# Optimization experiments

Measured on AMD Instinct MI355X. Metric: run time of the kernel, lower is better.

Reference implementation:

```python
import jax, jax.numpy as jnp
import numpy as np

B, S, D = 8, 4096, 1024  # batch, seq, input_dim == hidden_dim


def setup_inputs() -> dict:
    key = jax.random.key(0)
    k1, k2, k3, k4, k5 = jax.random.split(key, 5)
    s = 1.0 / np.sqrt(D)
    return {
        "q": jax.random.normal(k1, (B, S, D), dtype=jnp.float32),
        "k": jax.random.normal(k2, (B, D), dtype=jnp.float32),
        # torch Linear(in,out,bias=False) weight is [out,in]; store transposed [in,out]
        "W1": jax.random.uniform(k3, (D, D), dtype=jnp.float32, minval=-s, maxval=s),
        "W2": jax.random.uniform(k4, (D, D), dtype=jnp.float32, minval=-s, maxval=s),
        "V": jax.random.uniform(k5, (D, D), dtype=jnp.float32, minval=-s, maxval=s),
    }


def reference(q, k, W1, W2, V):
    # q: [B,S,D], k: [B,D]
    h_q = jnp.einsum("bsd,dh->bsh", q, W1)          # W1(q): [B,S,H]
    h_k = jnp.einsum("bd,dh->bh", k, W2)[:, None]   # W2(k).unsqueeze(1): [B,1,H]
    scores = jnp.einsum("bsh,hv->bsv", jnp.tanh(h_q + h_k), V)  # [B,S,H]
    weights = jax.nn.softmax(scores, axis=-1)       # softmax over feature dim (as in source)
    values = jnp.sum(weights * q, axis=1)           # [B,D]
    return values, weights
```

## Files before the change

### kernel.cpp

```cpp
#include <hip/hip_runtime.h>
#include <hip/hip_bf16.h>

#define DDIM 1024
#define BATCH 8
#define SEQ 4096
#define MROWS (BATCH*SEQ)

typedef __attribute__((ext_vector_type(8))) short short8;
typedef __attribute__((ext_vector_type(4))) float floatx4;

__device__ inline short f2bf(float f) {
    unsigned int u = __builtin_bit_cast(unsigned int, f);
    unsigned int r = (u + 0x7fffu + ((u >> 16) & 1u)) >> 16;
    return (short)r;
}
__device__ inline float bf2f(short s) {
    unsigned int u = ((unsigned int)(unsigned short)s) << 16;
    return __builtin_bit_cast(float, u);
}

__device__ inline float fast_tanh(float x) {
    float e = __expf(2.f * x);
    return 1.f - 2.f / (e + 1.f);
}

typedef const __attribute__((address_space(1))) unsigned int* gas_ptr;
typedef __attribute__((address_space(3))) unsigned int* las_ptr;
__device__ __forceinline__ void gl16(const short* g, short* l) {
    __builtin_amdgcn_global_load_lds((gas_ptr)g, (las_ptr)l, 16, 0, 0);
}

#define VMCNT4 asm volatile("s_waitcnt vmcnt(4)" ::: "memory")
#define VMCNT0 asm volatile("s_waitcnt vmcnt(0)" ::: "memory")
#define BARRIER do { __builtin_amdgcn_sched_barrier(0); __builtin_amdgcn_s_barrier(); \
                     __builtin_amdgcn_sched_barrier(0); } while (0)

__global__ __launch_bounds__(256) void prep_kernel(const float* __restrict__ q,
                                                   short* __restrict__ qb,
                                                   const float* __restrict__ W1,
                                                   short* __restrict__ W1T,
                                                   const float* __restrict__ V,
                                                   short* __restrict__ VT,
                                                   const float* __restrict__ k,
                                                   const float* __restrict__ W2,
                                                   float* __restrict__ hk) {
    int bid = blockIdx.x;
    if (bid < 2048) {
        size_t t = (size_t)bid * 256 + threadIdx.x;
        const size_t stride = (size_t)2048 * 256;
        for (int it = 0; it < 8; ++it, t += stride) {
            size_t i = t * 8;
            float4 f0 = *(const float4*)(q + i);
            float4 f1 = *(const float4*)(q + i + 4);
            short8 v;
            v[0]=f2bf(f0.x); v[1]=f2bf(f0.y); v[2]=f2bf(f0.z); v[3]=f2bf(f0.w);
            v[4]=f2bf(f1.x); v[5]=f2bf(f1.y); v[6]=f2bf(f1.z); v[7]=f2bf(f1.w);
            *(short8*)(qb + i) = v;
        }
    } else if (bid < 4096) {
        const float* src = (bid < 3072) ? W1 : V;
        short* dst = (bid < 3072) ? W1T : VT;
        int tb = (bid - 2048) & 1023;
        __shared__ float t[32][33];
        int bx = tb & 31, by = tb >> 5;
        int c  = threadIdx.x & 31;
        int r0 = threadIdx.x >> 5;
        for (int p = 0; p < 4; ++p) {
            int r = p * 8 + r0;
            t[r][c] = src[(size_t)(by * 32 + r) * DDIM + bx * 32 + c];
        }
        __syncthreads();
        for (int p = 0; p < 4; ++p) {
            int r = p * 8 + r0;
            dst[(size_t)(bx * 32 + r) * DDIM + by * 32 + c] = f2bf(t[c][r]);
        }
    } else {
        int hb = bid - 4096;
        int b  = hb >> 4;
        int h0 = (hb & 15) * 64;
        int hl = threadIdx.x & 63;
        int dc = threadIdx.x >> 6;
        const float* kb = k + (size_t)b * DDIM;
        float sum = 0.f;
        for (int d = dc * 256; d < dc * 256 + 256; ++d)
            sum += kb[d] * W2[(size_t)d * DDIM + h0 + hl];
        __shared__ float red[4][64];
        red[dc][hl] = sum;
        __syncthreads();
        if (dc == 0)
            hk[(size_t)b * DDIM + h0 + hl] = red[0][hl] + red[1][hl] + red[2][hl] + red[3][hl];
    }
}

template<int EPI>
__global__ __launch_bounds__(512, 2) void gemm256_kernel(const short* __restrict__ A,
                                                         const short* __restrict__ Bt,
                                                         const float* __restrict__ hk,
                                                         short* __restrict__ Out) {
    __shared__ __align__(16) short lds[2 * 32768];
    int bid = blockIdx.x;
    int swz = (bid & 7) * 64 + (bid >> 3);
    int mt = swz >> 2, nt = swz & 3;
    int m0 = mt * 256, n0 = nt * 256;
    int tid = threadIdx.x, lane = tid & 63, wid = tid >> 6;
    int wm = (wid >> 2) * 16;
    int wn = (wid & 3) * 16;
    int lr = lane & 15, kb = lane >> 4;
    floatx4 acc[8][4] = {};

    int srow = lane >> 3;
    int sblk = (lane & 7) ^ srow;
    const size_t arow_base = (size_t)(m0 + wid * 8 + srow) * DDIM + sblk * 8;
    const size_t brow_base = (size_t)(n0 + wid * 8 + srow) * DDIM + sblk * 8;
    const int lds_st = wid * 512 + lane * 8;

    auto stage = [&](int buf, int isB, int h, int t) {
        const short* src = isB ? Bt : A;
        size_t rb = isB ? brow_base : arow_base;
        #pragma unroll
        for (int r = 0; r < 2; ++r)
            gl16(src + rb + (size_t)(h * 128 + r * 64) * DDIM + t * 64,
                 lds + buf * 32768 + isB * 16384 + h * 8192 + r * 4096 + lds_st);
    };
    auto rdA = [&](int buf, int mi, int kk) -> short8 {
        int row = wm + mi * 32 + lr;
        return *(const short8*)(lds + buf * 32768 + (row >> 7) * 8192 +
                                (row & 127) * 64 + (((kk * 4 + kb) ^ (row & 7)) * 8));
    };
    auto rdB = [&](int buf, int ni, int kk) -> short8 {
        int row = wn + ni * 64 + lr;
        return *(const short8*)(lds + buf * 32768 + 16384 + (row >> 7) * 8192 +
                                (row & 127) * 64 + (((kk * 4 + kb) ^ (row & 7)) * 8));
    };

    stage(0, 0, 0, 0); stage(0, 1, 0, 0); stage(0, 1, 1, 0); stage(0, 0, 1, 0);
    VMCNT4;
    BARRIER;

    short8 a0[4][2], a1[4][2], b0[2][2], b1[2][2];

    for (int t = 0; t < 15; ++t) {
        int cb = t & 1, nb = cb ^ 1;
        stage(nb, 0, 0, t + 1);
        #pragma unroll
        for (int mi = 0; mi < 4; ++mi)
            #pragma unroll
            for (int kk = 0; kk < 2; ++kk) a0[mi][kk] = rdA(cb, mi, kk);
        #pragma unroll
        for (int ni = 0; ni < 2; ++ni)
            #pragma unroll
            for (int kk = 0; kk < 2; ++kk) b0[ni][kk] = rdB(cb, ni, kk);
        __builtin_amdgcn_s_setprio(1);
        #pragma unroll
        for (int mi = 0; mi < 4; ++mi)
            #pragma unroll
            for (int ni = 0; ni < 2; ++ni)
                #pragma unroll
                for (int kk = 0; kk < 2; ++kk)
                    acc[mi][ni] = __builtin_amdgcn_mfma_f32_16x16x32_bf16(a0[mi][kk], b0[ni][kk], acc[mi][ni], 0, 0, 0);
        __builtin_amdgcn_s_setprio(0);
        VMCNT4;
        BARRIER;
        stage(nb, 1, 0, t + 1);
        #pragma unroll
        for (int ni = 0; ni < 2; ++ni)
            #pragma unroll
            for (int kk = 0; kk < 2; ++kk) b1[ni][kk] = rdB(cb, ni + 2, kk);
        __builtin_amdgcn_s_setprio(1);
        #pragma unroll
        for (int mi = 0; mi < 4; ++mi)
            #pragma unroll
            for (int ni = 0; ni < 2; ++ni)
                #pragma unroll
                for (int kk = 0; kk < 2; ++kk)
                    acc[mi][ni + 2] = __builtin_amdgcn_mfma_f32_16x16x32_bf16(a0[mi][kk], b1[ni][kk], acc[mi][ni + 2], 0, 0, 0);
        __builtin_amdgcn_s_setprio(0);
        VMCNT4;
        BARRIER;
        stage(nb, 1, 1, t + 1);
        #pragma unroll
        for (int mi = 0; mi < 4; ++mi)
            #pragma unroll
            for (int kk = 0; kk < 2; ++kk) a1[mi][kk] = rdA(cb, mi + 4, kk);
        __builtin_amdgcn_s_setprio(1);
        #pragma unroll
        for (int mi = 0; mi < 4; ++mi)
            #pragma unroll
            for (int ni = 0; ni < 2; ++ni)
                #pragma unroll
                for (int kk = 0; kk < 2; ++kk)
                    acc[mi + 4][ni] = __builtin_amdgcn_mfma_f32_16x16x32_bf16(a1[mi][kk], b0[ni][kk], acc[mi + 4][ni], 0, 0, 0);
        __builtin_amdgcn_s_setprio(0);
        BARRIER;
        stage(nb, 0, 1, t + 1);
        __builtin_amdgcn_s_setprio(1);
        #pragma unroll
        for (int mi = 0; mi < 4; ++mi)
            #pragma unroll
            for (int ni = 0; ni < 2; ++ni)
                #pragma unroll
                for (int kk = 0; kk < 2; ++kk)
                    acc[mi + 4][ni + 2] = __builtin_amdgcn_mfma_f32_16x16x32_bf16(a1[mi][kk], b1[ni][kk], acc[mi + 4][ni + 2], 0, 0, 0);
        __builtin_amdgcn_s_setprio(0);
        VMCNT4;
        BARRIER;
    }

    {
        const int cb = 1;
        #pragma unroll
        for (int mi = 0; mi < 4; ++mi)
            #pragma unroll
            for (int kk = 0; kk < 2; ++kk) a0[mi][kk] = rdA(cb, mi, kk);
        #pragma unroll
        for (int ni = 0; ni < 2; ++ni)
            #pragma unroll
            for (int kk = 0; kk < 2; ++kk) b0[ni][kk] = rdB(cb, ni, kk);
        #pragma unroll
        for (int mi = 0; mi < 4; ++mi)
            #pragma unroll
            for (int ni = 0; ni < 2; ++ni)
                #pragma unroll
                for (int kk = 0; kk < 2; ++kk)
                    acc[mi][ni] = __builtin_amdgcn_mfma_f32_16x16x32_bf16(a0[mi][kk], b0[ni][kk], acc[mi][ni], 0, 0, 0);
        VMCNT0;
        BARRIER;
        #pragma unroll
        for (int ni = 0; ni < 2; ++ni)
            #pragma unroll
            for (int kk = 0; kk < 2; ++kk) b1[ni][kk] = rdB(cb, ni + 2, kk);
        #pragma unroll
        for (int mi = 0; mi < 4; ++mi)
            #pragma unroll
            for (int kk = 0; kk < 2; ++kk) a1[mi][kk] = rdA(cb, mi + 4, kk);
        #pragma unroll
        for (int mi = 0; mi < 4; ++mi)
            #pragma unroll
            for (int ni = 0; ni < 2; ++ni)
                #pragma unroll
                for (int kk = 0; kk < 2; ++kk) {
                    acc[mi][ni + 2]     = __builtin_amdgcn_mfma_f32_16x16x32_bf16(a0[mi][kk], b1[ni][kk], acc[mi][ni + 2], 0, 0, 0);
                    acc[mi + 4][ni]     = __builtin_amdgcn_mfma_f32_16x16x32_bf16(a1[mi][kk], b0[ni][kk], acc[mi + 4][ni], 0, 0, 0);
                    acc[mi + 4][ni + 2] = __builtin_amdgcn_mfma_f32_16x16x32_bf16(a1[mi][kk], b1[ni][kk], acc[mi + 4][ni + 2], 0, 0, 0);
                }
    }

    int rr = lane >> 4;
    if constexpr (EPI == 0) {
        int bidx = m0 >> 12;
        #pragma unroll
        for (int ni = 0; ni < 4; ++ni) {
            int col = n0 + wn + ni * 64 + lr;
            float hkv = hk[(size_t)bidx * DDIM + col];
            #pragma unroll
            for (int mi = 0; mi < 8; ++mi)
                #pragma unroll
                for (int j = 0; j < 4; ++j) {
                    int row = m0 + wm + mi * 32 + rr * 4 + j;
                    Out[(size_t)row * DDIM + col] = f2bf(fast_tanh(acc[mi][ni][j] + hkv));
                }
        }
    } else {
        #pragma unroll
        for (int ni = 0; ni < 4; ++ni) {
            int col = n0 + wn + ni * 64 + lr;
            #pragma unroll
            for (int mi = 0; mi < 8; ++mi)
                #pragma unroll
                for (int j = 0; j < 4; ++j) {
                    int row = m0 + wm + mi * 32 + rr * 4 + j;
                    Out[(size_t)row * DDIM + col] = f2bf(__expf(acc[mi][ni][j]));
                }
        }
    }
}

template<int QBF>
__global__ __launch_bounds__(256) void softmax_wsum_kernel(const short* __restrict__ E,
                                                           float* __restrict__ weights,
                                                           const float* __restrict__ q,
                                                           const short* __restrict__ qb,
                                                           float* __restrict__ partials) {
    int blk   = blockIdx.x;
    int b     = blk >> 8;
    int chunk = blk & 255;
    int tid   = threadIdx.x;
    int lane  = tid & 63, wid = tid >> 6;

    float pv[2][8] = {};
    size_t rowbase = ((size_t)b * SEQ + (size_t)chunk * 16 + (size_t)wid * 4) * DDIM;
    #pragma unroll 1
    for (int r = 0; r < 4; ++r) {
        const short* ep = E + rowbase + (size_t)r * DDIM;
        float x[2][8];
        float ls = 0.f;
        #pragma unroll
        for (int kk = 0; kk < 2; ++kk) {
            short8 v = *(const short8*)(ep + lane * 8 + kk * 512);
            #pragma unroll
            for (int j = 0; j < 8; ++j) { x[kk][j] = bf2f(v[j]); ls += x[kk][j]; }
        }
        #pragma unroll
        for (int o = 32; o > 0; o >>= 1) ls += __shfl_xor(ls, o);
        float inv = 1.f / ls;
        float* wp = weights + rowbase + (size_t)r * DDIM;
        #pragma unroll
        for (int kk = 0; kk < 2; ++kk) {
            int d = lane * 8 + kk * 512;
            float w[8];
            #pragma unroll
            for (int j = 0; j < 8; ++j) w[j] = x[kk][j] * inv;
            *(float4*)(wp + d)     = make_float4(w[0], w[1], w[2], w[3]);
            *(float4*)(wp + d + 4) = make_float4(w[4], w[5], w[6], w[7]);
            if constexpr (QBF) {
                short8 qv = *(const short8*)(qb + rowbase + (size_t)r * DDIM + d);
                #pragma unroll
                for (int j = 0; j < 8; ++j) pv[kk][j] += w[j] * bf2f(qv[j]);
            } else {
                const float* qp = q + rowbase + (size_t)r * DDIM;
                float4 q4a = *(const float4*)(qp + d);
                float4 q4b = *(const float4*)(qp + d + 4);
                pv[kk][0] += w[0] * q4a.x; pv[kk][1] += w[1] * q4a.y;
                pv[kk][2] += w[2] * q4a.z; pv[kk][3] += w[3] * q4a.w;
                pv[kk][4] += w[4] * q4b.x; pv[kk][5] += w[5] * q4b.y;
                pv[kk][6] += w[6] * q4b.z; pv[kk][7] += w[7] * q4b.w;
            }
        }
    }

    __shared__ float red[4][DDIM];
    #pragma unroll
    for (int kk = 0; kk < 2; ++kk) {
        int d = lane * 8 + kk * 512;
        *(float4*)(&red[wid][d])     = *(float4*)(&pv[kk][0]);
        *(float4*)(&red[wid][d + 4]) = *(float4*)(&pv[kk][4]);
    }
    __syncthreads();
    {
        int d = tid * 4;
        float4 s0 = *(float4*)(&red[0][d]);
        float4 s1 = *(float4*)(&red[1][d]);
        float4 s2 = *(float4*)(&red[2][d]);
        float4 s3 = *(float4*)(&red[3][d]);
        float4 o;
        o.x = s0.x + s1.x + s2.x + s3.x;
        o.y = s0.y + s1.y + s2.y + s3.y;
        o.z = s0.z + s1.z + s2.z + s3.z;
        o.w = s0.w + s1.w + s2.w + s3.w;
        *(float4*)(partials + (size_t)blk * DDIM + d) = o;
    }
}

__global__ __launch_bounds__(256) void reduce_values_kernel(const float* __restrict__ partials,
                                                            float* __restrict__ values) {
    int gid = blockIdx.x * 256 + threadIdx.x;
    int b = gid >> 10, v = gid & 1023;
    float s = 0.f;
    for (int c = 0; c < 256; ++c)
        s += partials[((size_t)b * 256 + c) * DDIM + v];
    values[gid] = s;
}

extern "C" void kernel_launch(void* const* d_in, const int* in_sizes, int n_in,
                              void* d_out, int out_size, void* d_ws, size_t ws_size,
                              hipStream_t stream) {
    const float* q  = (const float*)d_in[0];
    const float* k  = (const float*)d_in[1];
    const float* W1 = (const float*)d_in[2];
    const float* W2 = (const float*)d_in[3];
    const float* V  = (const float*)d_in[4];

    float* values  = (float*)d_out;
    float* weights = (float*)d_out + (size_t)BATCH * DDIM;

    const size_t hk_b   = (((size_t)BATCH * DDIM * 4) + 255) & ~(size_t)255;
    const size_t wT_b   = (size_t)DDIM * DDIM * 2;
    const size_t big_b  = (size_t)MROWS * DDIM * 2;
    const size_t part_b = (size_t)2048 * DDIM * 4;
    const size_t need_qbf_ws = hk_b + 2 * wT_b + 2 * big_b + part_b;

    char* ws = (char*)d_ws;
    float* hk  = (float*)ws;  ws += hk_b;
    short* W1T = (short*)ws;  ws += wT_b;
    short* VT  = (short*)ws;  ws += wT_b;
    short* E   = (short*)ws;  ws += big_b;

    short* q_bf;
    float* partials;
    bool qbf_in_ws = (ws_size >= need_qbf_ws);
    if (qbf_in_ws) {
        q_bf = (short*)ws;    ws += big_b;
        partials = (float*)ws;
    } else {
        q_bf = (short*)weights;
        partials = (float*)ws;
    }
    short* H = (short*)weights + (qbf_in_ws ? 0 : (size_t)MROWS * DDIM);

    prep_kernel<<<dim3(4224), dim3(256), 0, stream>>>(q, q_bf, W1, W1T, V, VT, k, W2, hk);
    gemm256_kernel<0><<<dim3(512), dim3(512), 0, stream>>>(q_bf, W1T, hk, H);
    gemm256_kernel<1><<<dim3(512), dim3(512), 0, stream>>>(H, VT, nullptr, E);
    if (qbf_in_ws)
        softmax_wsum_kernel<1><<<dim3(2048), dim3(256), 0, stream>>>(E, weights, q, q_bf, partials);
    else
        softmax_wsum_kernel<0><<<dim3(2048), dim3(256), 0, stream>>>(E, weights, q, q_bf, partials);
    reduce_values_kernel<<<dim3(32), dim3(256), 0, stream>>>(partials, values);
}
```

Measured before the change: 258.3 us.

## Fuse fp32-to-bf16 conversion of q into the first GEMM's A-tile loading

Removes the separate q bf16 conversion pass from the prep kernel. The first GEMM now loads fp32 q tiles into registers, converts them to bf16 and writes them into LDS itself. Blocks with nt==0 also store the converted tile to the q_bf buffer for later use by the softmax kernel. This saves one full read and write pass over q, but each A tile is read as fp32 four times (once per N tile), and the register-staged loads replace the async global-to-LDS path, which adds register pressure and changes pipelining.

Measured after the change: 269.4 us. +4.3%, slower.

```diff
diff --git a/kernel.cpp b/kernel.cpp
--- a/kernel.cpp
+++ b/kernel.cpp
@@ -18,6 +18,12 @@
     unsigned int u = ((unsigned int)(unsigned short)s) << 16;
     return __builtin_bit_cast(float, u);
 }
+__device__ inline short8 pack8(float4 a, float4 b) {
+    short8 v;
+    v[0]=f2bf(a.x); v[1]=f2bf(a.y); v[2]=f2bf(a.z); v[3]=f2bf(a.w);
+    v[4]=f2bf(b.x); v[5]=f2bf(b.y); v[6]=f2bf(b.z); v[7]=f2bf(b.w);
+    return v;
+}
 
 __device__ inline float fast_tanh(float x) {
     float e = __expf(2.f * x);
@@ -31,13 +37,13 @@
 }
 
 #define VMCNT4 asm volatile("s_waitcnt vmcnt(4)" ::: "memory")
+#define VMCNT6 asm volatile("s_waitcnt vmcnt(6)" ::: "memory")
 #define VMCNT0 asm volatile("s_waitcnt vmcnt(0)" ::: "memory")
+#define LGKM0  asm volatile("s_waitcnt lgkmcnt(0)" ::: "memory")
 #define BARRIER do { __builtin_amdgcn_sched_barrier(0); __builtin_amdgcn_s_barrier(); \
                      __builtin_amdgcn_sched_barrier(0); } while (0)
 
-__global__ __launch_bounds__(256) void prep_kernel(const float* __restrict__ q,
-                                                   short* __restrict__ qb,
-                                                   const float* __restrict__ W1,
+__global__ __launch_bounds__(256) void prep_kernel(const float* __restrict__ W1,
                                                    short* __restrict__ W1T,
                                                    const float* __restrict__ V,
                                                    short* __restrict__ VT,
@@ -46,21 +52,9 @@
                                                    float* __restrict__ hk) {
     int bid = blockIdx.x;
     if (bid < 2048) {
-        size_t t = (size_t)bid * 256 + threadIdx.x;
-        const size_t stride = (size_t)2048 * 256;
-        for (int it = 0; it < 8; ++it, t += stride) {
-            size_t i = t * 8;
-            float4 f0 = *(const float4*)(q + i);
-            float4 f1 = *(const float4*)(q + i + 4);
-            short8 v;
-            v[0]=f2bf(f0.x); v[1]=f2bf(f0.y); v[2]=f2bf(f0.z); v[3]=f2bf(f0.w);
-            v[4]=f2bf(f1.x); v[5]=f2bf(f1.y); v[6]=f2bf(f1.z); v[7]=f2bf(f1.w);
-            *(short8*)(qb + i) = v;
-        }
-    } else if (bid < 4096) {
-        const float* src = (bid < 3072) ? W1 : V;
-        short* dst = (bid < 3072) ? W1T : VT;
-        int tb = (bid - 2048) & 1023;
+        const float* src = (bid < 1024) ? W1 : V;
+        short* dst = (bid < 1024) ? W1T : VT;
+        int tb = bid & 1023;
         __shared__ float t[32][33];
         int bx = tb & 31, by = tb >> 5;
         int c  = threadIdx.x & 31;
@@ -75,7 +69,7 @@
             dst[(size_t)(bx * 32 + r) * DDIM + by * 32 + c] = f2bf(t[c][r]);
         }
     } else {
-        int hb = bid - 4096;
+        int hb = bid - 2048;
         int b  = hb >> 4;
         int h0 = (hb & 15) * 64;
         int hl = threadIdx.x & 63;
@@ -93,10 +87,11 @@
 }
 
 template<int EPI>
-__global__ __launch_bounds__(512, 2) void gemm256_kernel(const short* __restrict__ A,
+__global__ __launch_bounds__(512, 2) void gemm256_kernel(const void* __restrict__ Aptr,
                                                          const short* __restrict__ Bt,
                                                          const float* __restrict__ hk,
-                                                         short* __restrict__ Out) {
+                                                         short* __restrict__ Out,
+                                                         short* __restrict__ qbf) {
     __shared__ __align__(16) short lds[2 * 32768];
     int bid = blockIdx.x;
     int swz = (bid & 7) * 64 + (bid >> 3);
@@ -108,19 +103,46 @@
     int lr = lane & 15, kb = lane >> 4;
     floatx4 acc[8][4] = {};
 
+    const short* Abf = (const short*)Aptr;
+    const float* Af  = (const float*)Aptr;
+    const bool donate = (EPI == 0) && (nt == 0);
+
     int srow = lane >> 3;
     int sblk = (lane & 7) ^ srow;
     const size_t arow_base = (size_t)(m0 + wid * 8 + srow) * DDIM + sblk * 8;
     const size_t brow_base = (size_t)(n0 + wid * 8 + srow) * DDIM + sblk * 8;
     const int lds_st = wid * 512 + lane * 8;
 
-    auto stage = [&](int buf, int isB, int h, int t) {
-        const short* src = isB ? Bt : A;
-        size_t rb = isB ? brow_base : arow_base;
+    float4 fA0[2][2], fA1[2][2];
+
+    auto stageA16 = [&](int buf, int h, int t) {
         #pragma unroll
         for (int r = 0; r < 2; ++r)
-            gl16(src + rb + (size_t)(h * 128 + r * 64) * DDIM + t * 64,
-                 lds + buf * 32768 + isB * 16384 + h * 8192 + r * 4096 + lds_st);
+            gl16(Abf + arow_base + (size_t)(h * 128 + r * 64) * DDIM + t * 64,
+                 lds + buf * 32768 + h * 8192 + r * 4096 + lds_st);
+    };
+    auto stageB = [&](int buf, int h, int t) {
+        #pragma unroll
+        for (int r = 0; r < 2; ++r)
+            gl16(Bt + brow_base + (size_t)(h * 128 + r * 64) * DDIM + t * 64,
+                 lds + buf * 32768 + 16384 + h * 8192 + r * 4096 + lds_st);
+    };
+    auto loadA = [&](float4 (&f)[2][2], int h, int t) {
+        #pragma unroll
+        for (int r = 0; r < 2; ++r) {
+            const float* s = Af + arow_base + (size_t)(h * 128 + r * 64) * DDIM + t * 64;
+            f[r][0] = *(const float4*)s;
+            f[r][1] = *(const float4*)(s + 4);
+        }
+    };
+    auto writeA = [&](float4 (&f)[2][2], int buf, int h, int t) {
+        #pragma unroll
+        for (int r = 0; r < 2; ++r) {
+            short8 v = pack8(f[r][0], f[r][1]);
+            *(short8*)(lds + buf * 32768 + h * 8192 + r * 4096 + lds_st) = v;
+            if (donate)
+                *(short8*)(qbf + arow_base + (size_t)(h * 128 + r * 64) * DDIM + t * 64) = v;
+        }
     };
     auto rdA = [&](int buf, int mi, int kk) -> short8 {
         int row = wm + mi * 32 + lr;
@@ -133,15 +155,22 @@
                                 (row & 127) * 64 + (((kk * 4 + kb) ^ (row & 7)) * 8));
     };
 
-    stage(0, 0, 0, 0); stage(0, 1, 0, 0); stage(0, 1, 1, 0); stage(0, 0, 1, 0);
-    VMCNT4;
+    if constexpr (EPI == 0) {
+        loadA(fA0, 0, 0); stageB(0, 0, 0); stageB(0, 1, 0); loadA(fA1, 1, 0);
+        VMCNT6;
+        writeA(fA0, 0, 0, 0);
+        LGKM0;
+    } else {
+        stageA16(0, 0, 0); stageB(0, 0, 0); stageB(0, 1, 0); stageA16(0, 1, 0);
+        VMCNT4;
+    }
     BARRIER;
 
     short8 a0[4][2], a1[4][2], b0[2][2], b1[2][2];
 
     for (int t = 0; t < 15; ++t) {
         int cb = t & 1, nb = cb ^ 1;
-        stage(nb, 0, 0, t + 1);
+        if constexpr (EPI == 0) loadA(fA0, 0, t + 1); else stageA16(nb, 0, t + 1);
         #pragma unroll
         for (int mi = 0; mi < 4; ++mi)
             #pragma unroll
@@ -160,8 +189,9 @@
                     acc[mi][ni] = __builtin_amdgcn_mfma_f32_16x16x32_bf16(a0[mi][kk], b0[ni][kk], acc[mi][ni], 0, 0, 0);
         __builtin_amdgcn_s_setprio(0);
         VMCNT4;
+        if constexpr (EPI == 0) { writeA(fA1, cb, 1, t); LGKM0; }
         BARRIER;
-        stage(nb, 1, 0, t + 1);
+        stageB(nb, 0, t + 1);
         #pragma unroll
         for (int ni = 0; ni < 2; ++ni)
             #pragma unroll
@@ -175,9 +205,9 @@
                 for (int kk = 0; kk < 2; ++kk)
                     acc[mi][ni + 2] = __builtin_amdgcn_mfma_f32_16x16x32_bf16(a0[mi][kk], b1[ni][kk], acc[mi][ni + 2], 0, 0, 0);
         __builtin_amdgcn_s_setprio(0);
-        VMCNT4;
+        if constexpr (EPI == 1) VMCNT4;
         BARRIER;
-        stage(nb, 1, 1, t + 1);
+        stageB(nb, 1, t + 1);
         #pragma unroll
         for (int mi = 0; mi < 4; ++mi)
             #pragma unroll
@@ -192,7 +222,7 @@
                     acc[mi + 4][ni] = __builtin_amdgcn_mfma_f32_16x16x32_bf16(a1[mi][kk], b0[ni][kk], acc[mi + 4][ni], 0, 0, 0);
         __builtin_amdgcn_s_setprio(0);
         BARRIER;
-        stage(nb, 0, 1, t + 1);
+        if constexpr (EPI == 0) loadA(fA1, 1, t + 1); else stageA16(nb, 1, t + 1);
         __builtin_amdgcn_s_setprio(1);
         #pragma unroll
         for (int mi = 0; mi < 4; ++mi)
@@ -202,7 +232,13 @@
                 for (int kk = 0; kk < 2; ++kk)
                     acc[mi + 4][ni + 2] = __builtin_amdgcn_mfma_f32_16x16x32_bf16(a1[mi][kk], b1[ni][kk], acc[mi + 4][ni + 2], 0, 0, 0);
         __builtin_amdgcn_s_setprio(0);
-        VMCNT4;
+        if constexpr (EPI == 0) {
+            VMCNT6;
+            writeA(fA0, nb, 0, t + 1);
+            LGKM0;
+        } else {
+            VMCNT4;
+        }
         BARRIER;
     }
 
@@ -224,6 +260,7 @@
                 for (int kk = 0; kk < 2; ++kk)
                     acc[mi][ni] = __builtin_amdgcn_mfma_f32_16x16x32_bf16(a0[mi][kk], b0[ni][kk], acc[mi][ni], 0, 0, 0);
         VMCNT0;
+        if constexpr (EPI == 0) { writeA(fA1, cb, 1, 15); LGKM0; }
         BARRIER;
         #pragma unroll
         for (int ni = 0; ni < 2; ++ni)
@@ -397,9 +434,9 @@
     }
     short* H = (short*)weights + (qbf_in_ws ? 0 : (size_t)MROWS * DDIM);
 
-    prep_kernel<<<dim3(4224), dim3(256), 0, stream>>>(q, q_bf, W1, W1T, V, VT, k, W2, hk);
-    gemm256_kernel<0><<<dim3(512), dim3(512), 0, stream>>>(q_bf, W1T, hk, H);
-    gemm256_kernel<1><<<dim3(512), dim3(512), 0, stream>>>(H, VT, nullptr, E);
+    prep_kernel<<<dim3(2176), dim3(256), 0, stream>>>(W1, W1T, V, VT, k, W2, hk);
+    gemm256_kernel<0><<<dim3(512), dim3(512), 0, stream>>>((const void*)q, W1T, hk, H, q_bf);
+    gemm256_kernel<1><<<dim3(512), dim3(512), 0, stream>>>((const void*)H, VT, nullptr, E, nullptr);
     if (qbf_in_ws)
         softmax_wsum_kernel<1><<<dim3(2048), dim3(256), 0, stream>>>(E, weights, q, q_bf, partials);
     else
```
